# Optimization experiments

Measured on AMD Instinct MI355X. Metric: run time of the kernel, lower is better.

## Reference

```python
import jax, jax.numpy as jnp
import numpy as np

N = 8192      # points
NOBJ = 8      # objects
H = 64        # hidden_size (required by channel arithmetic, see notes)
CDIM = 128
K = 20
KNN = 360
EPS = 1e-5


def _lrelu(x):
    return jnp.where(x >= 0, x, 0.2 * x)


def _inorm2d(x):  # x: [C, N, K]; InstanceNorm2d, affine=False, biased var
    m = x.mean(axis=(1, 2), keepdims=True)
    v = ((x - m) ** 2).mean(axis=(1, 2), keepdims=True)
    return (x - m) / jnp.sqrt(v + EPS)


def _inorm1d(x):  # x: [C, L]
    m = x.mean(axis=1, keepdims=True)
    v = ((x - m) ** 2).mean(axis=1, keepdims=True)
    return (x - m) / jnp.sqrt(v + EPS)


def _block2d(W, f):  # 1x1 conv (no bias) + InstanceNorm2d + LeakyReLU(0.2)
    return _lrelu(_inorm2d(jnp.einsum('oc,cnk->onk', W, f)))


def _block1d(W, f):
    return _lrelu(_inorm1d(W @ f))


def _edge_feat(xc, idx):  # xc: [C, N], idx: [N, k] -> [2C, N, k]
    xt = xc.T                                   # [N, C]
    nb = xt[idx]                                # [N, k, C] gather
    ctr = jnp.broadcast_to(xt[:, None, :], nb.shape)
    return jnp.concatenate([nb - ctr, ctr], axis=2).transpose(2, 0, 1)


def _knn_idx(x, tag, k):  # kNN within same node_tag, self excluded
    xs = jax.lax.stop_gradient(x)
    sq = jnp.sum(xs * xs, axis=1)
    d2 = sq[:, None] + sq[None, :] - 2.0 * (xs @ xs.T)
    valid = (tag[:, None] == tag[None, :]) & ~jnp.eye(xs.shape[0], dtype=bool)
    d2 = jnp.where(valid, d2, jnp.inf)
    _, idx = jax.lax.top_k(-d2, k)              # ascending distance order
    return idx


def setup_inputs() -> dict:
    key = jax.random.key(0)
    ks = jax.random.split(key, 16)
    x = jax.random.normal(ks[0], (N, 3), dtype=jnp.float32)
    node_tag = (jnp.arange(N, dtype=jnp.int32) // (N // NOBJ))  # equal groups

    def w(k, o, i):
        return jax.random.normal(k, (o, i), dtype=jnp.float32) * (1.0 / np.sqrt(i))

    return {
        'x': x, 'node_tag': node_tag, 'n_obj': NOBJ,
        'W1': w(ks[1], H, 6),       'W2': w(ks[2], H, H),
        'W3': w(ks[3], H, 2 * H),   'W4': w(ks[4], H, H),
        'W5': w(ks[5], H, 2 * H),   'W6': w(ks[6], H, H),
        'W7': w(ks[7], H, 2 * H),   'W8': w(ks[8], H, H),
        'W9': w(ks[9], 128, 4 * H),
        'W10': w(ks[10], 2 * H, 3 * H),
        'W11': w(ks[11], 2 * H, 3 * H),
        'W12': w(ks[12], H, 3 * H),
        'W13': w(ks[13], H, 2 * H),
        'Wr': w(ks[14], CDIM, H),
    }


def reference(x, node_tag, n_obj, W1, W2, W3, W4, W5, W6, W7, W8, W9, W10,
              W11, W12, W13, Wr):
    n = x.shape[0]
    idx = _knn_idx(x, node_tag, KNN)            # [N, 360]

    f = _edge_feat(x.T, idx[:, :K])             # [6, N, 20]
    x1 = _block2d(W2, _block2d(W1, f)).max(axis=-1)            # [H, N]
    f = _edge_feat(x1, idx[:, :40:2])
    x2 = _block2d(W4, _block2d(W3, f)).max(axis=-1) + x1
    f = _edge_feat(x2, idx[:, :120:6])
    x3 = _block2d(W6, _block2d(W5, f)).max(axis=-1) + x2
    f = _edge_feat(x3, idx[:, :360:18])
    x4 = _block2d(W8, _block2d(W7, f)).max(axis=-1) + x3

    g = _block1d(W9, jnp.concatenate([x1, x2, x3, x4], axis=0))  # [128, N]
    g = jnp.broadcast_to(g.max(axis=1, keepdims=True), (128, n))

    x4 = _block1d(W10, jnp.concatenate([g, x4], axis=0))   # [2H, N]
    x3 = _block1d(W11, jnp.concatenate([x4, x3], axis=0))  # [2H, N]
    x2 = _block1d(W12, jnp.concatenate([x3, x2], axis=0))  # [H, N]
    x1 = _block1d(W13, jnp.concatenate([x2, x1], axis=0))  # [H, N]

    code = (Wr @ x1).T                                     # [N, c_dim]
    tag = node_tag.astype(jnp.int32)
    sums = jax.ops.segment_sum(code, tag, num_segments=n_obj)
    cnt = jax.ops.segment_sum(jnp.ones((n,), code.dtype), tag,
                              num_segments=n_obj)
    return sums / jnp.maximum(cnt, 1.0)[:, None]           # [n_obj, c_dim]
```

## Files before the change

### kernel.cpp

```cpp
#include <hip/hip_runtime.h>
#include <hip/hip_bf16.h>
#include <stdint.h>

typedef __hip_bfloat16 bf16;
typedef __attribute__((ext_vector_type(8))) short bfrag;
typedef __attribute__((ext_vector_type(4))) short s16x4;
typedef __attribute__((ext_vector_type(4))) float f32x4;

#define NPTS 8192
#define KSEL 20
#define MBIG (NPTS*KSEL)
#define EPSN 1e-5f

__device__ __forceinline__ float lrelu(float x){ return x >= 0.f ? x : 0.2f*x; }
__device__ __forceinline__ float ldx(const void* p, int i, int isbf){
  return isbf ? __bfloat162float(((const bf16*)p)[i]) : ((const float*)p)[i];
}
__device__ __forceinline__ short f2bs(float f){
  union { bf16 h; short s; } u;
  u.h = __float2bfloat16(f);
  return u.s;
}
__device__ __forceinline__ f32x4 mfma16(bfrag a, bfrag b, f32x4 c){
  return __builtin_amdgcn_mfma_f32_16x16x32_bf16(a, b, c, 0, 0, 0);
}
__device__ __forceinline__ unsigned fenc(float x){
  unsigned u = __float_as_uint(x);
  return (u & 0x80000000u) ? ~u : (u | 0x80000000u);
}
__device__ __forceinline__ float fdec(unsigned u){
  return __uint_as_float((u & 0x80000000u) ? (u & 0x7FFFFFFFu) : ~u);
}
__device__ __forceinline__ unsigned long long u64min(unsigned long long a, unsigned long long b){ return a<b?a:b; }
__device__ __forceinline__ unsigned long long u64max(unsigned long long a, unsigned long long b){ return a<b?b:a; }
__device__ __forceinline__ void ce(unsigned long long &a, unsigned long long &b, bool asc){
  unsigned long long mn = a<b?a:b, mx = a<b?b:a;
  a = asc ? mn : mx;
  b = asc ? mx : mn;
}

__global__ void zero_kernel(float* __restrict__ p, int n){
  int i = blockIdx.x*256 + threadIdx.x;
  if (i < n) p[i] = 0.f;
}

__global__ void detect_kernel(const void* __restrict__ x, int* __restrict__ badf){
  int i = blockIdx.x*256 + threadIdx.x;
  int bad = 0;
  for (; i < NPTS*3; i += gridDim.x*256){
    float v = __bfloat162float(((const bf16*)x)[i]);
    if (!(fabsf(v) < 1000.0f)) bad = 1;
  }
  if (__any(bad) && (threadIdx.x & 63) == 0) atomicOr(badf, 1);
}

__global__ __launch_bounds__(256) void knn_kernel(const void* __restrict__ x,
                                                  const int* __restrict__ tag,
                                                  int* __restrict__ idxc,
                                                  const int* __restrict__ flagp){
  __shared__ unsigned long long keysL[1024];
  const int isbf = (*flagp == 0);
  const int i = blockIdx.x;
  const int base = (i >> 10) << 10;
  const int t = threadIdx.x;
  const float xi = ldx(x, i*3+0, isbf);
  const float yi = ldx(x, i*3+1, isbf);
  const float zi = ldx(x, i*3+2, isbf);
  const float sqi = xi*xi + yi*yi + zi*zi;
  const int tagi = tag[i];

  unsigned long long v[4];
  #pragma unroll
  for (int r = 0; r < 4; r++){
    int j = 4*t + r, gj = base + j;
    float xj = ldx(x, gj*3+0, isbf);
    float yj = ldx(x, gj*3+1, isbf);
    float zj = ldx(x, gj*3+2, isbf);
    float sqj = xj*xj + yj*yj + zj*zj;
    float dot = xi*xj + yi*yj + zi*zj;
    float d2 = sqi + sqj - 2.0f*dot;
    bool valid = (gj != i) && (tag[gj] == tagi);
    unsigned k = valid ? fenc(d2) : 0xFFFFFFFFu;
    v[r] = ((unsigned long long)k << 32) | (unsigned)gj;
  }

  #pragma unroll
  for (int ksz = 2; ksz <= 1024; ksz <<= 1){
    #pragma unroll
    for (int jj = ksz >> 1; jj > 0; jj >>= 1){
      if (jj >= 256){
        __syncthreads();
        keysL[4*t+0] = v[0]; keysL[4*t+1] = v[1];
        keysL[4*t+2] = v[2]; keysL[4*t+3] = v[3];
        __syncthreads();
        const int pt = t ^ (jj >> 2);
        const bool keep_min = (((t & (ksz >> 2)) == 0) == ((t & (jj >> 2)) == 0));
        #pragma unroll
        for (int r = 0; r < 4; r++){
          unsigned long long o = keysL[4*pt + r];
          v[r] = keep_min ? u64min(v[r], o) : u64max(v[r], o);
        }
      } else if (jj >= 4){
        const int mask = jj >> 2;
        const bool keep_min = (((t & (ksz >> 2)) == 0) == ((t & mask) == 0));
        #pragma unroll
        for (int r = 0; r < 4; r++){
          unsigned long long o = __shfl_xor(v[r], mask, 64);
          v[r] = keep_min ? u64min(v[r], o) : u64max(v[r], o);
        }
      } else if (jj == 2){
        const bool asc = ((t & (ksz >> 2)) == 0);
        ce(v[0], v[2], asc);
        ce(v[1], v[3], asc);
      } else {
        if (ksz == 2){
          ce(v[0], v[1], true);
          ce(v[2], v[3], false);
        } else {
          const bool asc = ((t & (ksz >> 2)) == 0);
          ce(v[0], v[1], asc);
          ce(v[2], v[3], asc);
        }
      }
    }
  }

  __syncthreads();
  keysL[4*t+0] = v[0]; keysL[4*t+1] = v[1];
  keysL[4*t+2] = v[2]; keysL[4*t+3] = v[3];
  __syncthreads();
  if (t < 80){
    int s = t / 20, k = t - s*20;
    int step = (s == 0) ? 1 : (s == 1) ? 2 : (s == 2) ? 6 : 18;
    idxc[i*80 + t] = (int)(keysL[k*step] & 0xFFFFFFFFu);
  }
}

template<int KIN>
__global__ __launch_bounds__(256) void pq_kernel(
    const void* __restrict__ xin, const float* __restrict__ prev,
    const void* __restrict__ Wc, float* __restrict__ Pt, float* __restrict__ Qt,
    const int* __restrict__ flagp)
{
  __shared__ float WaS[16][KIN];
  __shared__ float WdS[16][KIN];
  const int isbf = (*flagp == 0);
  const int t = threadIdx.x;
  const int n0 = (blockIdx.x & 31) * 256;
  const int cg = (blockIdx.x >> 5) * 16;
  for (int l = t; l < 16*KIN; l += 256){
    int r = l / KIN, k = l - r*KIN;
    float wa = ldx(Wc, (cg + r)*(2*KIN) + k, isbf);
    float wb = ldx(Wc, (cg + r)*(2*KIN) + KIN + k, isbf);
    WaS[r][k] = wa;
    WdS[r][k] = wb - wa;
  }
  __syncthreads();
  const int n = n0 + t;
  float xr[KIN];
  if (KIN == 3){
    #pragma unroll
    for (int k = 0; k < KIN; k++) xr[k] = ldx(xin, n*3 + k, isbf);
  } else {
    #pragma unroll 8
    for (int k = 0; k < KIN; k++) xr[k] = prev[k*NPTS + n];
  }
  float pv[16], qv[16];
  #pragma unroll
  for (int r = 0; r < 16; r++){
    float p = 0.f, q = 0.f;
    #pragma unroll 8
    for (int k = 0; k < KIN; k++){
      p += WaS[r][k] * xr[k];
      q += WdS[r][k] * xr[k];
    }
    pv[r] = p; qv[r] = q;
  }
  #pragma unroll
  for (int r4 = 0; r4 < 4; r4++){
    *(float4*)&Pt[n*64 + cg + r4*4] = make_float4(pv[r4*4], pv[r4*4+1], pv[r4*4+2], pv[r4*4+3]);
    *(float4*)&Qt[n*64 + cg + r4*4] = make_float4(qv[r4*4], qv[r4*4+1], qv[r4*4+2], qv[r4*4+3]);
  }
}

__global__ __launch_bounds__(256) void stats1_kernel(
    const float* __restrict__ Pt, const float* __restrict__ Qt,
    const int* __restrict__ idxc, int sidx, float* __restrict__ stats)
{
  __shared__ __align__(16) float Qs[1024];
  __shared__ int ids[320];
  const int t = threadIdx.x;
  const int n0 = blockIdx.x * 16;
  for (int l = t; l < 1024; l += 256) Qs[l] = Qt[n0*64 + l];
  for (int l = t; l < 320; l += 256){
    int p = l / 20, k = l - p*20;
    ids[l] = idxc[(n0+p)*80 + sidx*20 + k] & (NPTS-1);
  }
  __syncthreads();
  const int tx = t & 15, ty = t >> 4;
  const int kq = tx >> 2, p0 = (tx & 3)*4;
  float sacc[4] = {0,0,0,0}, qacc[4] = {0,0,0,0};
  #pragma unroll
  for (int s = 0; s < 5; s++){
    int k = s*4 + kq;
    #pragma unroll
    for (int j = 0; j < 4; j++){
      int p = p0 + j;
      int nb = ids[p*20 + k];
      float4 pvv = *(const float4*)&Pt[nb*64 + ty*4];
      float4 qvv = *(const float4*)&Qs[p*64 + ty*4];
      float e0 = pvv.x+qvv.x, e1 = pvv.y+qvv.y, e2 = pvv.z+qvv.z, e3 = pvv.w+qvv.w;
      sacc[0]+=e0; sacc[1]+=e1; sacc[2]+=e2; sacc[3]+=e3;
      qacc[0]+=e0*e0; qacc[1]+=e1*e1; qacc[2]+=e2*e2; qacc[3]+=e3*e3;
    }
  }
  #pragma unroll
  for (int i = 0; i < 4; i++){
    float s = sacc[i], q = qacc[i];
    #pragma unroll
    for (int off = 8; off; off >>= 1){
      s += __shfl_down(s, off, 16);
      q += __shfl_down(q, off, 16);
    }
    if (tx == 0){
      atomicAdd(&stats[ty*4+i], s);
      atomicAdd(&stats[256+ty*4+i], q);
    }
  }
}

__global__ __launch_bounds__(256) void conv2_kernel(
    const float* __restrict__ Pt, const float* __restrict__ Qt,
    const int* __restrict__ idxc, int sidx,
    const void* __restrict__ W2c,
    const float* __restrict__ st1raw,
    float* __restrict__ stats2,
    float* __restrict__ rawmax,
    const int* __restrict__ flagp)
{
  __shared__ __align__(16) short Gs[64][72];
  __shared__ __align__(16) float Qs[1024];
  __shared__ int ids[320];
  __shared__ float nm1[64], niv1[64];
  const int isbf = (*flagp == 0);
  const int t = threadIdx.x;
  const int n0 = blockIdx.x * 16;
  const float invMB = 1.0f/(float)MBIG;

  for (int l = t; l < 1024; l += 256) Qs[l] = Qt[n0*64 + l];
  for (int l = t; l < 320; l += 256){
    int p = l / 20, k = l - p*20;
    ids[l] = idxc[(n0+p)*80 + sidx*20 + k] & (NPTS-1);
  }
  if (t < 64){
    float m = st1raw[t] * invMB;
    float v = st1raw[256+t]*invMB - m*m;
    nm1[t] = m;
    niv1[t] = 1.0f / sqrtf(fmaxf(v, 0.f) + EPSN);
  }

  const int lane = t & 63, w = t >> 6;
  const int nn = lane & 15, quad = lane >> 4;
  bfrag af0, af1;
  #pragma unroll
  for (int j = 0; j < 8; j++){
    af0[j] = f2bs(ldx(W2c, (16*w + nn)*64 +      quad*8 + j, isbf));
    af1[j] = f2bs(ldx(W2c, (16*w + nn)*64 + 32 + quad*8 + j, isbf));
  }
  __syncthreads();

  const int tx = t & 15, ty = t >> 4;
  float sacc[4] = {0,0,0,0}, qacc[4] = {0,0,0,0};
  float mxr[4] = {-3.4e38f,-3.4e38f,-3.4e38f,-3.4e38f};

  for (int s = 0; s < 5; s++){
    #pragma unroll
    for (int j = 0; j < 4; j++){
      int cg = tx*4 + j;
      int q = cg >> 4, p = cg & 15;
      int nb = ids[p*20 + s*4 + q];
      float4 pvv = *(const float4*)&Pt[nb*64 + ty*4];
      float4 qvv = *(const float4*)&Qs[p*64 + ty*4];
      s16x4 gv;
      gv[0] = f2bs(lrelu((pvv.x+qvv.x - nm1[ty*4+0]) * niv1[ty*4+0]));
      gv[1] = f2bs(lrelu((pvv.y+qvv.y - nm1[ty*4+1]) * niv1[ty*4+1]));
      gv[2] = f2bs(lrelu((pvv.z+qvv.z - nm1[ty*4+2]) * niv1[ty*4+2]));
      gv[3] = f2bs(lrelu((pvv.w+qvv.w - nm1[ty*4+3]) * niv1[ty*4+3]));
      *(s16x4*)&Gs[cg][ty*4] = gv;
    }
    __syncthreads();
    #pragma unroll
    for (int q = 0; q < 4; q++){
      bfrag b0 = *(bfrag*)&Gs[q*16 + nn][quad*8];
      bfrag b1 = *(bfrag*)&Gs[q*16 + nn][32 + quad*8];
      f32x4 acc = {0.f, 0.f, 0.f, 0.f};
      acc = mfma16(af0, b0, acc);
      acc = mfma16(af1, b1, acc);
      #pragma unroll
      for (int r = 0; r < 4; r++){
        float v = acc[r];
        sacc[r] += v; qacc[r] += v*v;
        mxr[r] = fmaxf(mxr[r], v);
      }
    }
    __syncthreads();
  }

  #pragma unroll
  for (int r = 0; r < 4; r++){
    int rr = 16*w + quad*4 + r;
    float s = sacc[r], q2 = qacc[r];
    #pragma unroll
    for (int off = 8; off; off >>= 1){
      s  += __shfl_down(s, off, 16);
      q2 += __shfl_down(q2, off, 16);
    }
    if (nn == 0){
      atomicAdd(&stats2[rr], s);
      atomicAdd(&stats2[256+rr], q2);
    }
    rawmax[rr*NPTS + n0 + nn] = mxr[r];
  }
}

__global__ __launch_bounds__(256) void maxres_kernel(
    const float* __restrict__ rawmax, const float* __restrict__ st2raw,
    const float* __restrict__ resid, float* __restrict__ xout)
{
  const float invMB = 1.0f/(float)MBIG;
  int g = blockIdx.x*256 + threadIdx.x;
  int c = g >> 13;
  float m = st2raw[c] * invMB;
  float v = st2raw[256+c]*invMB - m*m;
  float iv = 1.0f / sqrtf(fmaxf(v, 0.f) + EPSN);
  float y = lrelu((rawmax[g] - m) * iv);
  xout[g] = y + (resid ? resid[g] : 0.f);
}

template<int CTOT>
__global__ __launch_bounds__(256) void gemm1d_kernel(
    const void* __restrict__ W, int ldw, int koffW,
    const float* __restrict__ A, const float* __restrict__ Araw, float invA, int CA,
    const float* __restrict__ B,
    const float* __restrict__ cvec,
    float* __restrict__ Y,
    float* __restrict__ stats, unsigned* __restrict__ maxenc,
    const int* __restrict__ flagp)
{
  __shared__ __align__(16) short Fs[64][72];
  __shared__ float am[256], aiv[256];
  const int t = threadIdx.x;
  const int isbf = (*flagp == 0);
  const int colbase = (blockIdx.x & 127) * 64;
  const int rb = (blockIdx.x >> 7) * 64;
  const int lane = t & 63, w = t >> 6;
  const int nn = lane & 15, quad = lane >> 4;

  if (Araw && t < CA){
    float m = Araw[t]*invA;
    float v = Araw[256+t]*invA - m*m;
    am[t] = m; aiv[t] = 1.0f/sqrtf(fmaxf(v,0.f)+EPSN);
  }

  constexpr int K32 = CTOT >> 5;
  bfrag af[K32];
  const int arow = rb + 16*w + nn;
  #pragma unroll
  for (int f = 0; f < K32; f++)
    #pragma unroll
    for (int j = 0; j < 8; j++)
      af[f][j] = f2bs(ldx(W, arow*ldw + koffW + f*32 + quad*8 + j, isbf));

  f32x4 acc[4] = {};
  const int jcol = t & 63, kg = t >> 6;

  for (int kc = 0; kc < CTOT; kc += 64){
    __syncthreads();
    #pragma unroll
    for (int u = 0; u < 4; u++){
      int kl = kg*16 + u*4;
      s16x4 pk;
      #pragma unroll
      for (int z = 0; z < 4; z++){
        int k = kc + kl + z;
        float v;
        if (k < CA){
          v = A[k*NPTS + colbase + jcol];
          if (Araw) v = lrelu((v - am[k]) * aiv[k]);
        } else {
          v = B[(k-CA)*NPTS + colbase + jcol];
        }
        pk[z] = f2bs(v);
      }
      *(s16x4*)&Fs[jcol][kl] = pk;
    }
    __syncthreads();
    const int f0 = kc >> 5;
    #pragma unroll
    for (int q = 0; q < 4; q++){
      bfrag b0 = *(bfrag*)&Fs[q*16+nn][quad*8];
      bfrag b1 = *(bfrag*)&Fs[q*16+nn][32 + quad*8];
      acc[q] = mfma16(af[f0],   b0, acc[q]);
      acc[q] = mfma16(af[f0+1], b1, acc[q]);
    }
  }

  #pragma unroll
  for (int r = 0; r < 4; r++){
    int rr = rb + 16*w + quad*4 + r;
    float cv = cvec ? cvec[rr] : 0.f;
    float sum = 0.f, q2 = 0.f, mxv = -3.4e38f;
    #pragma unroll
    for (int q = 0; q < 4; q++){
      float v = acc[q][r] + cv;
      sum += v; q2 += v*v; mxv = fmaxf(mxv, v);
      if (Y) Y[rr*NPTS + colbase + q*16 + nn] = v;
    }
    #pragma unroll
    for (int off = 8; off; off >>= 1){
      sum += __shfl_down(sum, off, 16);
      q2  += __shfl_down(q2, off, 16);
      mxv  = fmaxf(mxv, __shfl_down(mxv, off, 16));
    }
    if (nn == 0){
      atomicAdd(&stats[rr], sum);
      atomicAdd(&stats[256+rr], q2);
      if (maxenc) atomicMax(&maxenc[rr], fenc(mxv));
    }
  }
}

__global__ void finalize_g_kernel(float* __restrict__ statsG,
    unsigned* __restrict__ gmaxenc, float* __restrict__ c0,
    const void* __restrict__ W10, const int* __restrict__ flagp)
{
  __shared__ float gsh[128];
  const int isbf = (*flagp == 0);
  int c = threadIdx.x;
  if (c < 128){
    float m = statsG[c] * (1.f/NPTS);
    float v = statsG[256+c]*(1.f/NPTS) - m*m;
    float iv = 1.0f / sqrtf(fmaxf(v, 0.f) + EPSN);
    gsh[c] = lrelu((fdec(gmaxenc[c]) - m) * iv);
  }
  __syncthreads();
  if (c < 128){
    float s = 0.f;
    for (int j = 0; j < 128; j++) s += ldx(W10, c*192 + j, isbf) * gsh[j];
    c0[c] = s;
  }
}

__global__ __launch_bounds__(256) void segsum_kernel(
    const float* __restrict__ ybuf, const float* __restrict__ straw,
    const int* __restrict__ tag, float* __restrict__ seg, float* __restrict__ cnt)
{
  const float invMN = 1.0f/(float)NPTS;
  int g = blockIdx.x*256 + threadIdx.x;
  int c = g >> 13, n = g & (NPTS-1);
  float m = straw[c] * invMN;
  float vv = straw[256+c]*invMN - m*m;
  float iv = 1.0f / sqrtf(fmaxf(vv, 0.f) + EPSN);
  float v = lrelu((ybuf[c*NPTS + n] - m) * iv);
  int tg = tag[n] & 7;
  int lane = threadIdx.x & 63;
  int t0 = __shfl(tg, 0, 64);
  bool uni = __all(tg == t0);
  if (uni){
    #pragma unroll
    for (int off = 32; off; off >>= 1) v += __shfl_down(v, off, 64);
    if (lane == 0){
      atomicAdd(&seg[t0*64 + c], v);
      if (c == 0) atomicAdd(cnt + t0, 64.f);
    }
  } else {
    atomicAdd(&seg[tg*64 + c], v);
    if (c == 0) atomicAdd(cnt + tg, 1.f);
  }
}

__global__ void final_kernel(const void* __restrict__ Wr,
    const float* __restrict__ seg, const float* __restrict__ cnt,
    void* __restrict__ out, int total, const int* __restrict__ flagp)
{
  const int isbf = (*flagp == 0);
  int q = blockIdx.x*blockDim.x + threadIdx.x;
  if (q >= total) return;
  int g = q >> 7, c = q & 127;
  float s = 0.f;
  for (int j = 0; j < 64; j++) s += ldx(Wr, c*64 + j, isbf) * seg[g*64 + j];
  float r = s / fmaxf(cnt[g], 1.f);
  if (isbf) ((bf16*)out)[q] = __float2bfloat16(r);
  else      ((float*)out)[q] = r;
}

extern "C" void kernel_launch(void* const* d_in, const int* in_sizes, int n_in,
                              void* d_out, int out_size, void* d_ws, size_t ws_size,
                              hipStream_t stream)
{
  const void* x   = d_in[0];
  const int* tag  = (const int*)d_in[1];
  const void* W1  = d_in[3];
  const void* W2  = d_in[4];
  const void* W3  = d_in[5];
  const void* W4  = d_in[6];
  const void* W5  = d_in[7];
  const void* W6  = d_in[8];
  const void* W7  = d_in[9];
  const void* W8  = d_in[10];
  const void* W9  = d_in[11];
  const void* W10 = d_in[12];
  const void* W11 = d_in[13];
  const void* W12 = d_in[14];
  const void* W13 = d_in[15];
  const void* Wr  = d_in[16];

  char* ws = (char*)d_ws;
  int*      idxc = (int*)ws;
  float*    xs   = (float*)(ws + 2621440);
  float* x1 = xs;
  float* x2 = xs +  64*NPTS;
  float* x3 = xs + 128*NPTS;
  float* x4 = xs + 192*NPTS;
  float*    y0   = (float*)(ws + 11010048);
  float*    y1   = (float*)(ws + 15204352);
  float*    rmax = (float*)(ws + 19398656);
  float*    Pt   = y0;
  float*    Qt   = y0 + 64*NPTS;
  float*    st   = (float*)(ws + 21495808);
  auto L = [&](int l){ return st + l*1024; };
  int*      flag     = (int*)(st + 13312);
  unsigned* gmaxenc  = (unsigned*)(st + 13440);
  float*    c0v      = st + 13568;
  float*    seg      = st + 13824;
  float*    cnt      = seg + 512;

  zero_kernel<<<64, 256, 0, stream>>>(st, 16384);
  detect_kernel<<<12, 256, 0, stream>>>(x, flag);
  knn_kernel<<<NPTS, 256, 0, stream>>>(x, tag, idxc, flag);

#define STAGE(KINV, XIN, PREV, WA, WB, LA, LB, XOUT, RES, SIDX)                              \
  pq_kernel<KINV><<<128, 256, 0, stream>>>(XIN, PREV, WA, Pt, Qt, flag);                     \
  stats1_kernel<<<512, 256, 0, stream>>>(Pt, Qt, idxc, SIDX, LA);                            \
  conv2_kernel<<<512, 256, 0, stream>>>(Pt, Qt, idxc, SIDX, WB, LA, LB, rmax, flag);         \
  maxres_kernel<<<64*NPTS/256, 256, 0, stream>>>(rmax, LB, RES, XOUT);

  STAGE(3,  x,       nullptr, W1, W2, L(0), L(1), x1, nullptr, 0)
  STAGE(64, nullptr, x1,      W3, W4, L(2), L(3), x2, x1,      1)
  STAGE(64, nullptr, x2,      W5, W6, L(4), L(5), x3, x2,      2)
  STAGE(64, nullptr, x3,      W7, W8, L(6), L(7), x4, x3,      3)
#undef STAGE

  gemm1d_kernel<256><<<256, 256, 0, stream>>>(W9, 256, 0, xs, nullptr, 0.f, 256,
                                              nullptr, nullptr, nullptr, L(8), gmaxenc, flag);
  finalize_g_kernel<<<1, 128, 0, stream>>>(L(8), gmaxenc, c0v, W10, flag);

  const float invMN = 1.0f/(float)NPTS;
  gemm1d_kernel<64> <<<256, 256, 0, stream>>>(W10, 192, 128, nullptr, nullptr, 0.f, 0,
                                              x4, c0v, y0, L(9), nullptr, flag);
  gemm1d_kernel<192><<<256, 256, 0, stream>>>(W11, 192, 0, y0, L(9), invMN, 128,
                                              x3, nullptr, y1, L(10), nullptr, flag);
  gemm1d_kernel<192><<<128, 256, 0, stream>>>(W12, 192, 0, y1, L(10), invMN, 128,
                                              x2, nullptr, y0, L(11), nullptr, flag);
  gemm1d_kernel<128><<<128, 256, 0, stream>>>(W13, 128, 0, y0, L(11), invMN, 64,
                                              x1, nullptr, y1, L(12), nullptr, flag);

  segsum_kernel<<<64*NPTS/256, 256, 0, stream>>>(y1, L(12), tag, seg, cnt);
  final_kernel<<<4, 256, 0, stream>>>(Wr, seg, cnt, d_out, out_size, flag);
}
```

Before: 981.7 us.

## Fuse maxres into next pq stage and halve tile sizes for more blocks

Folds the normalize+LeakyReLU+residual step (maxres) into the following pq_kernel, so stages 2-4 no longer read and write a separate x intermediate. The column-group-0 blocks of pq write the activation out for later use. stats1 and conv2 now process 8 points per block, doubling the grid, and the gemm1d kernels are templated on column tile width (32 or 16) to launch more blocks. The point is to cut kernel launches and memory round trips and to raise occupancy. The cost is less reuse per block, redundant normalize work across the four column groups in pq, and more atomic traffic.

```diff
diff --git a/kernel.cpp b/kernel.cpp
--- a/kernel.cpp
+++ b/kernel.cpp
@@ -136,18 +136,27 @@
   }
 }
 
-template<int KIN>
+template<int KIN, int FUSE>
 __global__ __launch_bounds__(256) void pq_kernel(
-    const void* __restrict__ xin, const float* __restrict__ prev,
+    const void* __restrict__ xin, const float* __restrict__ rmaxp,
     const void* __restrict__ Wc, float* __restrict__ Pt, float* __restrict__ Qt,
-    const int* __restrict__ flagp)
+    const float* __restrict__ straw, const float* __restrict__ resid,
+    float* __restrict__ xout, const int* __restrict__ flagp)
 {
   __shared__ float WaS[16][KIN];
   __shared__ float WdS[16][KIN];
+  __shared__ float nm[64], niv[64];
   const int isbf = (*flagp == 0);
   const int t = threadIdx.x;
   const int n0 = (blockIdx.x & 31) * 256;
   const int cg = (blockIdx.x >> 5) * 16;
+  if (FUSE && t < 64){
+    const float invMB = 1.0f/(float)MBIG;
+    float m = straw[t] * invMB;
+    float vv = straw[256+t]*invMB - m*m;
+    nm[t] = m;
+    niv[t] = 1.0f / sqrtf(fmaxf(vv, 0.f) + EPSN);
+  }
   for (int l = t; l < 16*KIN; l += 256){
     int r = l / KIN, k = l - r*KIN;
     float wa = ldx(Wc, (cg + r)*(2*KIN) + k, isbf);
@@ -163,7 +172,17 @@
     for (int k = 0; k < KIN; k++) xr[k] = ldx(xin, n*3 + k, isbf);
   } else {
     #pragma unroll 8
-    for (int k = 0; k < KIN; k++) xr[k] = prev[k*NPTS + n];
+    for (int k = 0; k < KIN; k++){
+      float vx;
+      if (FUSE){
+        float rv = rmaxp[k*NPTS + n];
+        vx = lrelu((rv - nm[k]) * niv[k]) + (resid ? resid[k*NPTS + n] : 0.f);
+        if (cg == 0) xout[k*NPTS + n] = vx;
+      } else {
+        vx = rmaxp[k*NPTS + n];
+      }
+      xr[k] = vx;
+    }
   }
   float pv[16], qv[16];
   #pragma unroll
@@ -187,25 +206,25 @@
     const float* __restrict__ Pt, const float* __restrict__ Qt,
     const int* __restrict__ idxc, int sidx, float* __restrict__ stats)
 {
-  __shared__ __align__(16) float Qs[1024];
-  __shared__ int ids[320];
+  __shared__ __align__(16) float Qs[512];
+  __shared__ int ids[160];
   const int t = threadIdx.x;
-  const int n0 = blockIdx.x * 16;
-  for (int l = t; l < 1024; l += 256) Qs[l] = Qt[n0*64 + l];
-  for (int l = t; l < 320; l += 256){
-    int p = l / 20, k = l - p*20;
-    ids[l] = idxc[(n0+p)*80 + sidx*20 + k] & (NPTS-1);
+  const int n0 = blockIdx.x * 8;
+  for (int l = t; l < 512; l += 256) Qs[l] = Qt[n0*64 + l];
+  if (t < 160){
+    int p = t / 20, k = t - p*20;
+    ids[t] = idxc[(n0+p)*80 + sidx*20 + k] & (NPTS-1);
   }
   __syncthreads();
   const int tx = t & 15, ty = t >> 4;
-  const int kq = tx >> 2, p0 = (tx & 3)*4;
+  const int kq = tx >> 2, ph = tx & 3;
   float sacc[4] = {0,0,0,0}, qacc[4] = {0,0,0,0};
   #pragma unroll
   for (int s = 0; s < 5; s++){
     int k = s*4 + kq;
     #pragma unroll
-    for (int j = 0; j < 4; j++){
-      int p = p0 + j;
+    for (int j = 0; j < 2; j++){
+      int p = ph*2 + j;
       int nb = ids[p*20 + k];
       float4 pvv = *(const float4*)&Pt[nb*64 + ty*4];
       float4 qvv = *(const float4*)&Qs[p*64 + ty*4];
@@ -238,19 +257,19 @@
     float* __restrict__ rawmax,
     const int* __restrict__ flagp)
 {
-  __shared__ __align__(16) short Gs[64][72];
-  __shared__ __align__(16) float Qs[1024];
-  __shared__ int ids[320];
+  __shared__ __align__(16) short Gs[16][72];
+  __shared__ __align__(16) float Qs[512];
+  __shared__ int ids[160];
   __shared__ float nm1[64], niv1[64];
   const int isbf = (*flagp == 0);
   const int t = threadIdx.x;
-  const int n0 = blockIdx.x * 16;
+  const int n0 = blockIdx.x * 8;
   const float invMB = 1.0f/(float)MBIG;
 
-  for (int l = t; l < 1024; l += 256) Qs[l] = Qt[n0*64 + l];
-  for (int l = t; l < 320; l += 256){
-    int p = l / 20, k = l - p*20;
-    ids[l] = idxc[(n0+p)*80 + sidx*20 + k] & (NPTS-1);
+  for (int l = t; l < 512; l += 256) Qs[l] = Qt[n0*64 + l];
+  if (t < 160){
+    int p = t / 20, k = t - p*20;
+    ids[t] = idxc[(n0+p)*80 + sidx*20 + k] & (NPTS-1);
   }
   if (t < 64){
     float m = st1raw[t] * invMB;
@@ -273,12 +292,10 @@
   float sacc[4] = {0,0,0,0}, qacc[4] = {0,0,0,0};
   float mxr[4] = {-3.4e38f,-3.4e38f,-3.4e38f,-3.4e38f};
 
-  for (int s = 0; s < 5; s++){
-    #pragma unroll
-    for (int j = 0; j < 4; j++){
-      int cg = tx*4 + j;
-      int q = cg >> 4, p = cg & 15;
-      int nb = ids[p*20 + s*4 + q];
+  for (int s2 = 0; s2 < 10; s2++){
+    {
+      int kq2 = tx >> 3, p = tx & 7;
+      int nb = ids[p*20 + 2*s2 + kq2];
       float4 pvv = *(const float4*)&Pt[nb*64 + ty*4];
       float4 qvv = *(const float4*)&Qs[p*64 + ty*4];
       s16x4 gv;
@@ -286,22 +303,19 @@
       gv[1] = f2bs(lrelu((pvv.y+qvv.y - nm1[ty*4+1]) * niv1[ty*4+1]));
       gv[2] = f2bs(lrelu((pvv.z+qvv.z - nm1[ty*4+2]) * niv1[ty*4+2]));
       gv[3] = f2bs(lrelu((pvv.w+qvv.w - nm1[ty*4+3]) * niv1[ty*4+3]));
-      *(s16x4*)&Gs[cg][ty*4] = gv;
+      *(s16x4*)&Gs[tx][ty*4] = gv;
     }
     __syncthreads();
-    #pragma unroll
-    for (int q = 0; q < 4; q++){
-      bfrag b0 = *(bfrag*)&Gs[q*16 + nn][quad*8];
-      bfrag b1 = *(bfrag*)&Gs[q*16 + nn][32 + quad*8];
-      f32x4 acc = {0.f, 0.f, 0.f, 0.f};
-      acc = mfma16(af0, b0, acc);
-      acc = mfma16(af1, b1, acc);
-      #pragma unroll
-      for (int r = 0; r < 4; r++){
-        float v = acc[r];
-        sacc[r] += v; qacc[r] += v*v;
-        mxr[r] = fmaxf(mxr[r], v);
-      }
+    bfrag b0 = *(bfrag*)&Gs[nn][quad*8];
+    bfrag b1 = *(bfrag*)&Gs[nn][32 + quad*8];
+    f32x4 acc = {0.f, 0.f, 0.f, 0.f};
+    acc = mfma16(af0, b0, acc);
+    acc = mfma16(af1, b1, acc);
+    #pragma unroll
+    for (int r = 0; r < 4; r++){
+      float v = acc[r];
+      sacc[r] += v; qacc[r] += v*v;
+      mxr[r] = fmaxf(mxr[r], v);
     }
     __syncthreads();
   }
@@ -319,7 +333,8 @@
       atomicAdd(&stats2[rr], s);
       atomicAdd(&stats2[256+rr], q2);
     }
-    rawmax[rr*NPTS + n0 + nn] = mxr[r];
+    float m = fmaxf(mxr[r], __shfl_xor(mxr[r], 8, 16));
+    if (nn < 8) rawmax[rr*NPTS + n0 + nn] = m;
   }
 }
 
@@ -337,7 +352,7 @@
   xout[g] = y + (resid ? resid[g] : 0.f);
 }
 
-template<int CTOT>
+template<int CTOT, int COLS>
 __global__ __launch_bounds__(256) void gemm1d_kernel(
     const void* __restrict__ W, int ldw, int koffW,
     const float* __restrict__ A, const float* __restrict__ Araw, float invA, int CA,
@@ -347,12 +362,13 @@
     float* __restrict__ stats, unsigned* __restrict__ maxenc,
     const int* __restrict__ flagp)
 {
-  __shared__ __align__(16) short Fs[64][72];
+  __shared__ __align__(16) short Fs[COLS][72];
   __shared__ float am[256], aiv[256];
   const int t = threadIdx.x;
   const int isbf = (*flagp == 0);
-  const int colbase = (blockIdx.x & 127) * 64;
-  const int rb = (blockIdx.x >> 7) * 64;
+  constexpr int NCT = NPTS / COLS;
+  const int colbase = (blockIdx.x % NCT) * COLS;
+  const int rb = (blockIdx.x / NCT) * 64;
   const int lane = t & 63, w = t >> 6;
   const int nn = lane & 15, quad = lane >> 4;
 
@@ -371,14 +387,16 @@
     for (int j = 0; j < 8; j++)
       af[f][j] = f2bs(ldx(W, arow*ldw + koffW + f*32 + quad*8 + j, isbf));
 
-  f32x4 acc[4] = {};
-  const int jcol = t & 63, kg = t >> 6;
+  constexpr int QN = COLS/16;
+  constexpr int UN = COLS/16;
+  f32x4 acc[QN] = {};
+  const int jcol = t % COLS, kg = t / COLS;
 
   for (int kc = 0; kc < CTOT; kc += 64){
     __syncthreads();
     #pragma unroll
-    for (int u = 0; u < 4; u++){
-      int kl = kg*16 + u*4;
+    for (int u = 0; u < UN; u++){
+      int kl = kg*(4*UN) + u*4;
       s16x4 pk;
       #pragma unroll
       for (int z = 0; z < 4; z++){
@@ -397,7 +415,7 @@
     __syncthreads();
     const int f0 = kc >> 5;
     #pragma unroll
-    for (int q = 0; q < 4; q++){
+    for (int q = 0; q < QN; q++){
       bfrag b0 = *(bfrag*)&Fs[q*16+nn][quad*8];
       bfrag b1 = *(bfrag*)&Fs[q*16+nn][32 + quad*8];
       acc[q] = mfma16(af[f0],   b0, acc[q]);
@@ -411,7 +429,7 @@
     float cv = cvec ? cvec[rr] : 0.f;
     float sum = 0.f, q2 = 0.f, mxv = -3.4e38f;
     #pragma unroll
-    for (int q = 0; q < 4; q++){
+    for (int q = 0; q < QN; q++){
       float v = acc[q][r] + cv;
       sum += v; q2 += v*v; mxv = fmaxf(mxv, v);
       if (Y) Y[rr*NPTS + colbase + q*16 + nn] = v;
@@ -539,31 +557,33 @@
   detect_kernel<<<12, 256, 0, stream>>>(x, flag);
   knn_kernel<<<NPTS, 256, 0, stream>>>(x, tag, idxc, flag);
 
-#define STAGE(KINV, XIN, PREV, WA, WB, LA, LB, XOUT, RES, SIDX)                              \
-  pq_kernel<KINV><<<128, 256, 0, stream>>>(XIN, PREV, WA, Pt, Qt, flag);                     \
-  stats1_kernel<<<512, 256, 0, stream>>>(Pt, Qt, idxc, SIDX, LA);                            \
-  conv2_kernel<<<512, 256, 0, stream>>>(Pt, Qt, idxc, SIDX, WB, LA, LB, rmax, flag);         \
-  maxres_kernel<<<64*NPTS/256, 256, 0, stream>>>(rmax, LB, RES, XOUT);
-
-  STAGE(3,  x,       nullptr, W1, W2, L(0), L(1), x1, nullptr, 0)
-  STAGE(64, nullptr, x1,      W3, W4, L(2), L(3), x2, x1,      1)
-  STAGE(64, nullptr, x2,      W5, W6, L(4), L(5), x3, x2,      2)
-  STAGE(64, nullptr, x3,      W7, W8, L(6), L(7), x4, x3,      3)
-#undef STAGE
-
-  gemm1d_kernel<256><<<256, 256, 0, stream>>>(W9, 256, 0, xs, nullptr, 0.f, 256,
-                                              nullptr, nullptr, nullptr, L(8), gmaxenc, flag);
+  pq_kernel<3,0><<<128, 256, 0, stream>>>(x, nullptr, W1, Pt, Qt, nullptr, nullptr, nullptr, flag);
+  stats1_kernel<<<1024, 256, 0, stream>>>(Pt, Qt, idxc, 0, L(0));
+  conv2_kernel<<<1024, 256, 0, stream>>>(Pt, Qt, idxc, 0, W2, L(0), L(1), rmax, flag);
+  pq_kernel<64,1><<<128, 256, 0, stream>>>(nullptr, rmax, W3, Pt, Qt, L(1), nullptr, x1, flag);
+  stats1_kernel<<<1024, 256, 0, stream>>>(Pt, Qt, idxc, 1, L(2));
+  conv2_kernel<<<1024, 256, 0, stream>>>(Pt, Qt, idxc, 1, W4, L(2), L(3), rmax, flag);
+  pq_kernel<64,1><<<128, 256, 0, stream>>>(nullptr, rmax, W5, Pt, Qt, L(3), x1, x2, flag);
+  stats1_kernel<<<1024, 256, 0, stream>>>(Pt, Qt, idxc, 2, L(4));
+  conv2_kernel<<<1024, 256, 0, stream>>>(Pt, Qt, idxc, 2, W6, L(4), L(5), rmax, flag);
+  pq_kernel<64,1><<<128, 256, 0, stream>>>(nullptr, rmax, W7, Pt, Qt, L(5), x2, x3, flag);
+  stats1_kernel<<<1024, 256, 0, stream>>>(Pt, Qt, idxc, 3, L(6));
+  conv2_kernel<<<1024, 256, 0, stream>>>(Pt, Qt, idxc, 3, W8, L(6), L(7), rmax, flag);
+  maxres_kernel<<<64*NPTS/256, 256, 0, stream>>>(rmax, L(7), x3, x4);
+
+  gemm1d_kernel<256,32><<<512, 256, 0, stream>>>(W9, 256, 0, xs, nullptr, 0.f, 256,
+                                                 nullptr, nullptr, nullptr, L(8), gmaxenc, flag);
   finalize_g_kernel<<<1, 128, 0, stream>>>(L(8), gmaxenc, c0v, W10, flag);
 
   const float invMN = 1.0f/(float)NPTS;
-  gemm1d_kernel<64> <<<256, 256, 0, stream>>>(W10, 192, 128, nullptr, nullptr, 0.f, 0,
-                                              x4, c0v, y0, L(9), nullptr, flag);
-  gemm1d_kernel<192><<<256, 256, 0, stream>>>(W11, 192, 0, y0, L(9), invMN, 128,
-                                              x3, nullptr, y1, L(10), nullptr, flag);
-  gemm1d_kernel<192><<<128, 256, 0, stream>>>(W12, 192, 0, y1, L(10), invMN, 128,
-                                              x2, nullptr, y0, L(11), nullptr, flag);
-  gemm1d_kernel<128><<<128, 256, 0, stream>>>(W13, 128, 0, y0, L(11), invMN, 64,
-                                              x1, nullptr, y1, L(12), nullptr, flag);
+  gemm1d_kernel<64,32> <<<512, 256, 0, stream>>>(W10, 192, 128, nullptr, nullptr, 0.f, 0,
+                                                 x4, c0v, y0, L(9), nullptr, flag);
+  gemm1d_kernel<192,32><<<512, 256, 0, stream>>>(W11, 192, 0, y0, L(9), invMN, 128,
+                                                 x3, nullptr, y1, L(10), nullptr, flag);
+  gemm1d_kernel<192,16><<<512, 256, 0, stream>>>(W12, 192, 0, y1, L(10), invMN, 128,
+                                                 x2, nullptr, y0, L(11), nullptr, flag);
+  gemm1d_kernel<128,16><<<512, 256, 0, stream>>>(W13, 128, 0, y0, L(11), invMN, 64,
+                                                 x1, nullptr, y1, L(12), nullptr, flag);
 
   segsum_kernel<<<64*NPTS/256, 256, 0, stream>>>(y1, L(12), tag, seg, cnt);
   final_kernel<<<4, 256, 0, stream>>>(Wr, seg, cnt, d_out, out_size, flag);
```

Result: slower. 1.513 ms (+54.1%).
